# Kernel optimization log

Hardware: AMD Instinct MI355X
Metric: run time of the kernel (lower is better)

The kernel has to match this reference:

```python
import jax, jax.numpy as jnp
import numpy as np

N, NFEAT, NHID, NCLASS, NHEADS = 8192, 512, 64, 16, 4
ALPHA = 0.2          # leaky_relu slope for attention scores
OUT_SLOPE = 0.01     # flax default slope for per-head output leaky_relu
NEG = -9000000000000000.0


def glorot(key, shape):
    fan_in, fan_out = shape[0], shape[1]
    lim = jnp.sqrt(6.0 / (fan_in + fan_out))
    return jax.random.uniform(key, shape, jnp.float32, -lim, lim)


def setup_inputs() -> dict:
    key = jax.random.key(0)
    ks = jax.random.split(key, 6)
    x = jax.random.normal(ks[0], (N, NFEAT), jnp.float32)
    adj = jax.random.randint(ks[1], (N, N), 0, 2, jnp.int32)
    Wh = glorot(ks[2], (NHEADS * NFEAT, NHID)).reshape(NHEADS, NFEAT, NHID)
    ah = glorot(ks[3], (NHEADS * 2 * NHID, 1)).reshape(NHEADS, 2 * NHID, 1)
    Wo = glorot(ks[4], (NHID * NHEADS, NCLASS))
    ao = glorot(ks[5], (2 * NCLASS, 1))
    return {"x": x, "adj": adj, "Wh": Wh, "ah": ah, "Wo": Wo, "ao": ao}


def _gat_layer(x, adj_mask, W, a, score_slope):
    # h: (N, F)
    h = x @ W
    F = h.shape[1]
    # a_input[i,j] = concat(h_i, h_j); a_input @ a == f1[i] + f2[j]
    f1 = h @ a[:F, 0]   # (N,)
    f2 = h @ a[F:, 0]   # (N,)
    e = jax.nn.leaky_relu(f1[:, None] + f2[None, :], negative_slope=score_slope)
    att = jax.nn.softmax(jnp.where(adj_mask, e, NEG), axis=1)  # (N, N)
    return att @ h  # (N, F)


def reference(x, adj, Wh, ah, Wo, ao):
    adj_mask = adj > 0
    heads = []
    for k in range(NHEADS):  # small fixed structural loop
        hp = _gat_layer(x, adj_mask, Wh[k], ah[k], ALPHA)
        heads.append(jax.nn.leaky_relu(hp, negative_slope=OUT_SLOPE))
    xcat = jnp.concatenate(heads, axis=1)  # (N, NHEADS*NHID)
    # output head: concat=False -> return h_prime directly
    return _gat_layer(xcat, adj_mask, Wo, ao, ALPHA)  # (N, NCLASS)
```

## Files before the change

kernel.cpp:

```cpp
#include <hip/hip_runtime.h>
#include <stdint.h>

#define N      8192
#define FEAT   512
#define HID    64
#define NH     4
#define C1     256
#define PCH    80
#define TC     320
#define NCLS   16
#define C2     32
#define IPB    8

typedef __attribute__((ext_vector_type(8))) short bf16x8;
typedef __attribute__((ext_vector_type(4))) float f32x4;

__device__ __forceinline__ float b2f(uint16_t u){
  uint32_t x = ((uint32_t)u) << 16;
  return __builtin_bit_cast(float, x);
}
__device__ __forceinline__ uint16_t f2b(float f){
  uint32_t x = __builtin_bit_cast(uint32_t, f);
  uint32_t r = (x + 0x7fffu + ((x >> 16) & 1u)) >> 16;
  return (uint16_t)r;
}
__device__ __forceinline__ float lrelu(float v, float a){ return fmaxf(v, a * v); }

__global__ void k0_wht(const float* __restrict__ Wh, float* __restrict__ WhT){
  int idx = blockIdx.x * 256 + threadIdx.x;
  int k = idx >> 15;
  int r = idx & 32767;
  int cc = r >> 9, f = r & 511;
  WhT[idx] = Wh[k * 32768 + f * 64 + cc];
}

__global__ __launch_bounds__(256) void k1_h(const float* __restrict__ x,
    const float* __restrict__ WhT, const float* __restrict__ ah,
    uint16_t* __restrict__ H, float* __restrict__ f1, float* __restrict__ f2)
{
  __shared__ float4 xs[IPB][128];
  int t = threadIdx.x;
  int i0 = blockIdx.x * IPB;
  for (int r = t; r < IPB * 128; r += 256){
    int ii = r >> 7, o = r & 127;
    xs[ii][o] = *((const float4*)(x + (size_t)(i0 + ii) * FEAT) + o);
  }
  __syncthreads();
  int k = t >> 6, cc = t & 63;
  const float4* wrow = (const float4*)(WhT + k * 32768 + cc * 512);
  float acc[IPB] = {};
  for (int f4 = 0; f4 < 128; ++f4){
    float4 wv = wrow[f4];
    #pragma unroll
    for (int ii = 0; ii < IPB; ++ii){
      float4 xv = xs[ii][f4];
      acc[ii] += xv.x * wv.x + xv.y * wv.y + xv.z * wv.z + xv.w * wv.w;
    }
  }
  float a1 = ah[k * 128 + cc], a2 = ah[k * 128 + 64 + cc];
  #pragma unroll
  for (int ii = 0; ii < IPB; ++ii){
    int i = i0 + ii;
    H[(size_t)i * C1 + t] = f2b(acc[ii]);
    float c1v = acc[ii] * a1, c2v = acc[ii] * a2;
    #pragma unroll
    for (int off = 32; off; off >>= 1){
      c1v += __shfl_down(c1v, off);
      c2v += __shfl_down(c2v, off);
    }
    if (cc == 0){ f1[k * N + i] = c1v; f2[k * N + i] = c2v; }
  }
}

__global__ void k2a_htT(const uint16_t* __restrict__ H, uint16_t* __restrict__ HT){
  __shared__ uint16_t tile[64][65];
  int bid = blockIdx.x;
  int k = bid & 3, it = bid >> 2;
  int i0 = it * 64;
  int t = threadIdx.x;
  #pragma unroll
  for (int r = 0; r < 4; ++r){
    int ii = r * 16 + (t >> 4);
    int pp = (t & 15) * 4;
    uint2 v = *(const uint2*)(H + (size_t)(i0 + ii) * C1 + k * 64 + pp);
    const uint16_t* s = (const uint16_t*)&v;
    tile[pp + 0][ii] = s[0]; tile[pp + 1][ii] = s[1];
    tile[pp + 2][ii] = s[2]; tile[pp + 3][ii] = s[3];
  }
  __syncthreads();
  #pragma unroll
  for (int r = 0; r < 4; ++r){
    int pp = r * 16 + (t >> 4);
    int ii = (t & 15) * 4;
    uint2 v;
    uint16_t* s = (uint16_t*)&v;
    s[0] = tile[pp][ii + 0]; s[1] = tile[pp][ii + 1];
    s[2] = tile[pp][ii + 2]; s[3] = tile[pp][ii + 3];
    *(uint2*)(HT + (size_t)k * (PCH * N) + (size_t)pp * N + i0 + ii) = v;
  }
}

__global__ void k2b_fill(uint16_t* __restrict__ HT){
  int fidx = blockIdx.x * 256 + threadIdx.x;
  int k = fidx >> 14;
  int rem = fidx & 16383;
  int p = 64 + (rem >> 10);
  int i0 = (rem & 1023) << 3;
  uint32_t w = (p == 64) ? 0x3F803F80u : 0u;
  uint4 v = {w, w, w, w};
  *((uint4*)(HT + (size_t)k * (PCH * N) + (size_t)p * N + i0)) = v;
}

__global__ __launch_bounds__(256, 2) void k3_attA(const int* __restrict__ adj,
    const uint16_t* __restrict__ HT, const float* __restrict__ f1,
    const float* __restrict__ f2, float* __restrict__ accA)
{
  __shared__ uint16_t Pl[NH][64][48];
  __shared__ uint16_t Hl[TC][48];
  __shared__ float f1s[NH][64];

  const int t = threadIdx.x;
  const int ibl = blockIdx.x >> 2;
  const int js = blockIdx.x & 3;
  const int gi0 = ibl * 64;

  { int k = t >> 6, ii = t & 63; f1s[k][ii] = f1[k * N + gi0 + ii]; }

  const int tj   = t & 31;
  const int half = t >> 5;
  const int lane = t & 63;
  const int wid  = t >> 6;
  const int m    = lane & 15;
  const int q    = lane >> 4;

  f32x4 acc[4][5] = {};
  const int* arow0 = adj + (size_t)(gi0 + half) * N + tj;

  for (int jc = 0; jc < 64; ++jc){
    const int gj = js * 2048 + jc * 32;
    float f2v0 = f2[0 * N + gj + tj];
    float f2v1 = f2[1 * N + gj + tj];
    float f2v2 = f2[2 * N + gj + tj];
    float f2v3 = f2[3 * N + gj + tj];
    int av[8];
    #pragma unroll
    for (int r = 0; r < 8; ++r) av[r] = arow0[(size_t)(8 * r) * N + gj];

    __syncthreads();
    #pragma unroll
    for (int r = 0; r < 5; ++r){
      int idx = t + 256 * r;
      int p = idx >> 2, o4 = idx & 3;
      *(uint4*)&Hl[p][o4 * 8] = *(const uint4*)(HT + (size_t)p * N + gj + o4 * 8);
    }
    #pragma unroll
    for (int r = 0; r < 8; ++r){
      int i = half + 8 * r;
      int a = av[r];
      float s0 = f1s[0][i] + f2v0;
      float s1 = f1s[1][i] + f2v1;
      float s2 = f1s[2][i] + f2v2;
      float s3 = f1s[3][i] + f2v3;
      float w0 = (a > 0) ? __expf(lrelu(s0, 0.2f)) : 0.f;
      float w1 = (a > 0) ? __expf(lrelu(s1, 0.2f)) : 0.f;
      float w2 = (a > 0) ? __expf(lrelu(s2, 0.2f)) : 0.f;
      float w3 = (a > 0) ? __expf(lrelu(s3, 0.2f)) : 0.f;
      Pl[0][i][tj] = f2b(w0);
      Pl[1][i][tj] = f2b(w1);
      Pl[2][i][tj] = f2b(w2);
      Pl[3][i][tj] = f2b(w3);
    }
    __syncthreads();

    bf16x8 af[4];
    #pragma unroll
    for (int it = 0; it < 4; ++it)
      af[it] = *(const bf16x8*)&Pl[wid][it * 16 + m][q * 8];
    #pragma unroll
    for (int ct = 0; ct < 5; ++ct){
      bf16x8 bfr = *(const bf16x8*)&Hl[wid * PCH + ct * 16 + m][q * 8];
      #pragma unroll
      for (int it = 0; it < 4; ++it)
        acc[it][ct] = __builtin_amdgcn_mfma_f32_16x16x32_bf16(af[it], bfr, acc[it][ct], 0, 0, 0);
    }
  }

  #pragma unroll
  for (int it = 0; it < 4; ++it)
    #pragma unroll
    for (int ct = 0; ct < 5; ++ct)
      #pragma unroll
      for (int reg = 0; reg < 4; ++reg){
        int gi = gi0 + it * 16 + q * 4 + reg;
        int c  = wid * PCH + ct * 16 + m;
        accA[((size_t)js * N + gi) * TC + c] = acc[it][ct][reg];
      }
}

__global__ void k4_redA(const float* __restrict__ accA, uint16_t* __restrict__ xcat){
  int i = blockIdx.x;
  int t = threadIdx.x;
  int k = t >> 6, cc = t & 63;
  size_t base = (size_t)i * TC + k * PCH;
  float v = 0.f, Z = 0.f;
  #pragma unroll
  for (int js = 0; js < 4; ++js){
    const float* p = accA + (size_t)js * N * TC + base;
    v += p[cc];
    Z += p[64];
  }
  float r = v / Z;
  xcat[(size_t)i * C1 + t] = f2b(lrelu(r, 0.01f));
}

__global__ __launch_bounds__(256) void k5_h2(const uint16_t* __restrict__ xcat,
    const float* __restrict__ Wo, const float* __restrict__ ao,
    uint16_t* __restrict__ h2T, float* __restrict__ f1o, float* __restrict__ f2o)
{
  __shared__ uint16_t xs[16][256];
  int t = threadIdx.x;
  int i0 = blockIdx.x * 16;
  #pragma unroll
  for (int r = 0; r < 2; ++r){
    int idx = t + 256 * r;
    int ii = idx >> 5, o4 = idx & 31;
    *(uint4*)&xs[ii][o4 * 8] = *(const uint4*)(xcat + (size_t)(i0 + ii) * C1 + o4 * 8);
  }
  __syncthreads();
  int ii = t >> 4, c = t & 15;
  float acc = 0.f;
  for (int f = 0; f < 256; ++f)
    acc += b2f(xs[ii][f]) * Wo[f * 16 + c];
  int i = i0 + ii;
  h2T[(size_t)c * N + i] = f2b(acc);
  float u1 = acc * ao[c];
  float u2 = acc * ao[16 + c];
  #pragma unroll
  for (int off = 8; off; off >>= 1){
    u1 += __shfl_down(u1, off, 16);
    u2 += __shfl_down(u2, off, 16);
  }
  if (c == 0){ f1o[i] = u1; f2o[i] = u2; }
  if (t < 16) h2T[(size_t)16 * N + i0 + t] = 0x3F80;
  if (t < 240){
    int p = 17 + t / 16, io = t % 16;
    h2T[(size_t)p * N + i0 + io] = 0;
  }
}

__global__ __launch_bounds__(256) void k6_attB(const int* __restrict__ adj,
    const uint16_t* __restrict__ h2T, const float* __restrict__ f1o,
    const float* __restrict__ f2o, float* __restrict__ accB)
{
  __shared__ uint16_t Pl[64][48];
  __shared__ uint16_t Hl[32][48];
  __shared__ float f1s[64];

  const int t = threadIdx.x;
  const int ibl = blockIdx.x >> 3;
  const int js = blockIdx.x & 7;
  const int gi0 = ibl * 64;
  if (t < 64) f1s[t] = f1o[gi0 + t];

  const int tj = t & 31;
  const int half = t >> 5;
  const int lane = t & 63;
  const int wid = t >> 6;
  const int m = lane & 15;
  const int q = lane >> 4;

  f32x4 acc0 = {0.f, 0.f, 0.f, 0.f}, acc1 = {0.f, 0.f, 0.f, 0.f};
  const int* arow0 = adj + (size_t)(gi0 + half) * N + tj;

  for (int jc = 0; jc < 32; ++jc){
    const int gj = js * 1024 + jc * 32;
    float f2v = f2o[gj + tj];
    int av[8];
    #pragma unroll
    for (int r = 0; r < 8; ++r) av[r] = arow0[(size_t)(8 * r) * N + gj];

    __syncthreads();
    if (t < 128){
      int p = t >> 2, o4 = t & 3;
      *(uint4*)&Hl[p][o4 * 8] = *(const uint4*)(h2T + (size_t)p * N + gj + o4 * 8);
    }
    #pragma unroll
    for (int r = 0; r < 8; ++r){
      int i = half + 8 * r;
      float s = f1s[i] + f2v;
      float w = (av[r] > 0) ? __expf(lrelu(s, 0.2f)) : 0.f;
      Pl[i][tj] = f2b(w);
    }
    __syncthreads();

    bf16x8 af = *(const bf16x8*)&Pl[wid * 16 + m][q * 8];
    bf16x8 b0 = *(const bf16x8*)&Hl[m][q * 8];
    bf16x8 b1 = *(const bf16x8*)&Hl[16 + m][q * 8];
    acc0 = __builtin_amdgcn_mfma_f32_16x16x32_bf16(af, b0, acc0, 0, 0, 0);
    acc1 = __builtin_amdgcn_mfma_f32_16x16x32_bf16(af, b1, acc1, 0, 0, 0);
  }

  #pragma unroll
  for (int reg = 0; reg < 4; ++reg){
    int gi = gi0 + wid * 16 + q * 4 + reg;
    accB[((size_t)js * N + gi) * C2 + m] = acc0[reg];
    accB[((size_t)js * N + gi) * C2 + 16 + m] = acc1[reg];
  }
}

__global__ void k7_redB(const float* __restrict__ accB, float* __restrict__ out){
  int idx = blockIdx.x * 256 + threadIdx.x;
  int i = idx >> 4, c = idx & 15;
  float v = 0.f, Z = 0.f;
  #pragma unroll
  for (int js = 0; js < 8; ++js){
    const float* p = accB + ((size_t)js * N + i) * C2;
    v += p[c];
    Z += p[16];
  }
  out[idx] = v / Z;
}

extern "C" void kernel_launch(void* const* d_in, const int* in_sizes, int n_in,
                              void* d_out, int out_size, void* d_ws, size_t ws_size,
                              hipStream_t stream)
{
  const float* x   = (const float*)d_in[0];
  const int*   adj = (const int*)d_in[1];
  const float* Wh  = (const float*)d_in[2];
  const float* ah  = (const float*)d_in[3];
  const float* Wo  = (const float*)d_in[4];
  const float* ao  = (const float*)d_in[5];
  float* out = (float*)d_out;

  char* ws = (char*)d_ws;
  float*    WhT  = (float*)   (ws);
  uint16_t* H    = (uint16_t*)(ws + 524288);
  uint16_t* HT   = (uint16_t*)(ws + 4718592);
  float*    f1   = (float*)   (ws + 9961472);
  float*    f2   = (float*)   (ws + 10092544);
  float*    accA = (float*)   (ws + 10223616);
  uint16_t* xcat = (uint16_t*)(ws + 52166656);
  uint16_t* h2T  = (uint16_t*)(ws + 56360960);
  float*    f1o  = (float*)   (ws + 56885248);
  float*    f2o  = (float*)   (ws + 56918016);
  float*    accB = (float*)   (ws + 56950784);

  hipLaunchKernelGGL(k0_wht,   dim3(512),  dim3(256), 0, stream, Wh, WhT);
  hipLaunchKernelGGL(k1_h,     dim3(1024), dim3(256), 0, stream, x, WhT, ah, H, f1, f2);
  hipLaunchKernelGGL(k2a_htT,  dim3(512),  dim3(256), 0, stream, H, HT);
  hipLaunchKernelGGL(k2b_fill, dim3(256),  dim3(256), 0, stream, HT);
  hipLaunchKernelGGL(k3_attA,  dim3(512),  dim3(256), 0, stream, adj, HT, f1, f2, accA);
  hipLaunchKernelGGL(k4_redA,  dim3(8192), dim3(256), 0, stream, accA, xcat);
  hipLaunchKernelGGL(k5_h2,    dim3(512),  dim3(256), 0, stream, xcat, Wo, ao, h2T, f1o, f2o);
  hipLaunchKernelGGL(k6_attB,  dim3(1024), dim3(256), 0, stream, adj, h2T, f1o, f2o, accB);
  hipLaunchKernelGGL(k7_redB,  dim3(512),  dim3(256), 0, stream, accB, out);
}
```

Measured before the change: 630.9 us.

## Pipeline attention loads, compute softmax denominators in VALU, double block size

Both attention kernels now prefetch the next chunk's H tile, adjacency values and f2 scores into registers while computing the current chunk, using A/B register buffers. The softmax row sums are accumulated in registers and reduced with shuffles, replacing the padded ones-column in HT and dropping the fill kernel and its MFMA columns. Scores are pre-scaled by log2(e) so a native exp2 can be used, and bf16 packing goes through v_cvt_pk_bf16_f32. The first attention kernel goes to 512 threads with a head-by-row-tile wave split. The denominator is now summed from fp32 weights rather than bf16-rounded ones, which slightly changes numerics, and the extra prefetch registers may raise register pressure.

```diff
diff --git a/kernel.cpp b/kernel.cpp
--- a/kernel.cpp
+++ b/kernel.cpp
@@ -11,6 +11,7 @@
 #define NCLS   16
 #define C2     32
 #define IPB    8
+#define LOG2E  1.44269504f
 
 typedef __attribute__((ext_vector_type(8))) short bf16x8;
 typedef __attribute__((ext_vector_type(4))) float f32x4;
@@ -25,6 +26,18 @@
   return (uint16_t)r;
 }
 __device__ __forceinline__ float lrelu(float v, float a){ return fmaxf(v, a * v); }
+__device__ __forceinline__ float fexp2(float x){
+#if __has_builtin(__builtin_amdgcn_exp2f)
+  return __builtin_amdgcn_exp2f(x);
+#else
+  return exp2f(x);
+#endif
+}
+__device__ __forceinline__ uint32_t pk_bf16(float lo, float hi){
+  uint32_t r;
+  asm("v_cvt_pk_bf16_f32 %0, %1, %2" : "=v"(r) : "v"(lo), "v"(hi));
+  return r;
+}
 
 __global__ void k0_wht(const float* __restrict__ Wh, float* __restrict__ WhT){
   int idx = blockIdx.x * 256 + threadIdx.x;
@@ -68,7 +81,7 @@
       c1v += __shfl_down(c1v, off);
       c2v += __shfl_down(c2v, off);
     }
-    if (cc == 0){ f1[k * N + i] = c1v; f2[k * N + i] = c2v; }
+    if (cc == 0){ f1[k * N + i] = c1v * LOG2E; f2[k * N + i] = c2v * LOG2E; }
   }
 }
 
@@ -96,27 +109,55 @@
     uint16_t* s = (uint16_t*)&v;
     s[0] = tile[pp][ii + 0]; s[1] = tile[pp][ii + 1];
     s[2] = tile[pp][ii + 2]; s[3] = tile[pp][ii + 3];
-    *(uint2*)(HT + (size_t)k * (PCH * N) + (size_t)pp * N + i0 + ii) = v;
-  }
-}
-
-__global__ void k2b_fill(uint16_t* __restrict__ HT){
-  int fidx = blockIdx.x * 256 + threadIdx.x;
-  int k = fidx >> 14;
-  int rem = fidx & 16383;
-  int p = 64 + (rem >> 10);
-  int i0 = (rem & 1023) << 3;
-  uint32_t w = (p == 64) ? 0x3F803F80u : 0u;
-  uint4 v = {w, w, w, w};
-  *((uint4*)(HT + (size_t)k * (PCH * N) + (size_t)p * N + i0)) = v;
-}
-
-__global__ __launch_bounds__(256, 2) void k3_attA(const int* __restrict__ adj,
+    *(uint2*)(HT + (size_t)k * (64 * N) + (size_t)pp * N + i0 + ii) = v;
+  }
+}
+
+#define K3_BODY(JC, CUR, NXT)                                                    \
+  {                                                                              \
+    __syncthreads();                                                             \
+    *(uint4*)&Hl[p0][o40 * 8] = h##CUR##0;                                       \
+    *(uint4*)&Hl[p1][o40 * 8] = h##CUR##1;                                       \
+    const int gjn = js * 2048 + (((JC) + 1) & 63) * 32;                          \
+    h##NXT##0 = *(const uint4*)(src0 + gjn);                                     \
+    h##NXT##1 = *(const uint4*)(src1 + gjn);                                     \
+    _Pragma("unroll")                                                            \
+    for (int r = 0; r < 4; ++r) av##NXT[r] = arow[(size_t)(16 * r) * N + gjn];   \
+    _Pragma("unroll")                                                            \
+    for (int k = 0; k < 4; ++k) f##NXT[k] = f2[(size_t)k * N + gjn + tj];        \
+    _Pragma("unroll")                                                            \
+    for (int r = 0; r < 4; ++r){                                                 \
+      const int i = half + 16 * r;                                               \
+      const int a = av##CUR[r];                                                  \
+      float e0, e1, e2, e3;                                                      \
+      { float s = f1s[0][i] + f##CUR[0]; e0 = fexp2(fmaxf(s, 0.2f * s)); }       \
+      { float s = f1s[1][i] + f##CUR[1]; e1 = fexp2(fmaxf(s, 0.2f * s)); }       \
+      { float s = f1s[2][i] + f##CUR[2]; e2 = fexp2(fmaxf(s, 0.2f * s)); }       \
+      { float s = f1s[3][i] + f##CUR[3]; e3 = fexp2(fmaxf(s, 0.2f * s)); }       \
+      if (a <= 0){ e0 = 0.f; e1 = 0.f; e2 = 0.f; e3 = 0.f; }                     \
+      dsum[0][r] += e0; dsum[1][r] += e1;                                        \
+      dsum[2][r] += e2; dsum[3][r] += e3;                                        \
+      uint32_t pk01 = pk_bf16(e0, e1), pk23 = pk_bf16(e2, e3);                   \
+      Pl[0][i][tj] = (uint16_t)pk01; Pl[1][i][tj] = (uint16_t)(pk01 >> 16);      \
+      Pl[2][i][tj] = (uint16_t)pk23; Pl[3][i][tj] = (uint16_t)(pk23 >> 16);      \
+    }                                                                            \
+    __syncthreads();                                                             \
+    bf16x8 af0 = *(const bf16x8*)&Pl[head][(ith * 2 + 0) * 16 + m][q * 8];       \
+    bf16x8 af1 = *(const bf16x8*)&Pl[head][(ith * 2 + 1) * 16 + m][q * 8];       \
+    _Pragma("unroll")                                                            \
+    for (int ct = 0; ct < 4; ++ct){                                              \
+      bf16x8 bfr = *(const bf16x8*)&Hl[head * 64 + ct * 16 + m][q * 8];          \
+      acc[0][ct] = __builtin_amdgcn_mfma_f32_16x16x32_bf16(af0, bfr, acc[0][ct], 0, 0, 0); \
+      acc[1][ct] = __builtin_amdgcn_mfma_f32_16x16x32_bf16(af1, bfr, acc[1][ct], 0, 0, 0); \
+    }                                                                            \
+  }
+
+__global__ __launch_bounds__(512, 4) void k3_attA(const int* __restrict__ adj,
     const uint16_t* __restrict__ HT, const float* __restrict__ f1,
     const float* __restrict__ f2, float* __restrict__ accA)
 {
-  __shared__ uint16_t Pl[NH][64][48];
-  __shared__ uint16_t Hl[TC][48];
+  __shared__ uint16_t Pl[NH][64][40];
+  __shared__ uint16_t Hl[256][40];
   __shared__ float f1s[NH][64];
 
   const int t = threadIdx.x;
@@ -124,77 +165,67 @@
   const int js = blockIdx.x & 3;
   const int gi0 = ibl * 64;
 
-  { int k = t >> 6, ii = t & 63; f1s[k][ii] = f1[k * N + gi0 + ii]; }
+  if (t < 256){ int k = t >> 6, ii = t & 63; f1s[k][ii] = f1[k * N + gi0 + ii]; }
 
   const int tj   = t & 31;
   const int half = t >> 5;
   const int lane = t & 63;
-  const int wid  = t >> 6;
+  const int w    = t >> 6;
+  const int head = w >> 1;
+  const int ith  = w & 1;
   const int m    = lane & 15;
   const int q    = lane >> 4;
 
-  f32x4 acc[4][5] = {};
-  const int* arow0 = adj + (size_t)(gi0 + half) * N + tj;
-
-  for (int jc = 0; jc < 64; ++jc){
-    const int gj = js * 2048 + jc * 32;
-    float f2v0 = f2[0 * N + gj + tj];
-    float f2v1 = f2[1 * N + gj + tj];
-    float f2v2 = f2[2 * N + gj + tj];
-    float f2v3 = f2[3 * N + gj + tj];
-    int av[8];
-    #pragma unroll
-    for (int r = 0; r < 8; ++r) av[r] = arow0[(size_t)(8 * r) * N + gj];
-
-    __syncthreads();
-    #pragma unroll
-    for (int r = 0; r < 5; ++r){
-      int idx = t + 256 * r;
-      int p = idx >> 2, o4 = idx & 3;
-      *(uint4*)&Hl[p][o4 * 8] = *(const uint4*)(HT + (size_t)p * N + gj + o4 * 8);
-    }
-    #pragma unroll
-    for (int r = 0; r < 8; ++r){
-      int i = half + 8 * r;
-      int a = av[r];
-      float s0 = f1s[0][i] + f2v0;
-      float s1 = f1s[1][i] + f2v1;
-      float s2 = f1s[2][i] + f2v2;
-      float s3 = f1s[3][i] + f2v3;
-      float w0 = (a > 0) ? __expf(lrelu(s0, 0.2f)) : 0.f;
-      float w1 = (a > 0) ? __expf(lrelu(s1, 0.2f)) : 0.f;
-      float w2 = (a > 0) ? __expf(lrelu(s2, 0.2f)) : 0.f;
-      float w3 = (a > 0) ? __expf(lrelu(s3, 0.2f)) : 0.f;
-      Pl[0][i][tj] = f2b(w0);
-      Pl[1][i][tj] = f2b(w1);
-      Pl[2][i][tj] = f2b(w2);
-      Pl[3][i][tj] = f2b(w3);
-    }
-    __syncthreads();
-
-    bf16x8 af[4];
-    #pragma unroll
-    for (int it = 0; it < 4; ++it)
-      af[it] = *(const bf16x8*)&Pl[wid][it * 16 + m][q * 8];
-    #pragma unroll
-    for (int ct = 0; ct < 5; ++ct){
-      bf16x8 bfr = *(const bf16x8*)&Hl[wid * PCH + ct * 16 + m][q * 8];
-      #pragma unroll
-      for (int it = 0; it < 4; ++it)
-        acc[it][ct] = __builtin_amdgcn_mfma_f32_16x16x32_bf16(af[it], bfr, acc[it][ct], 0, 0, 0);
-    }
-  }
-
-  #pragma unroll
-  for (int it = 0; it < 4; ++it)
-    #pragma unroll
-    for (int ct = 0; ct < 5; ++ct)
+  const int p0 = t >> 2, o40 = t & 3;
+  const int p1 = p0 + 128;
+  const uint16_t* src0 = HT + (size_t)p0 * N + o40 * 8;
+  const uint16_t* src1 = HT + (size_t)p1 * N + o40 * 8;
+
+  f32x4 acc[2][4] = {};
+  float dsum[NH][4] = {};
+  const int* arow = adj + (size_t)(gi0 + half) * N + tj;
+
+  uint4 hA0, hA1, hB0, hB1;
+  int avA[4], avB[4];
+  float fA[4], fB[4];
+
+  {
+    const int gj0 = js * 2048;
+    hA0 = *(const uint4*)(src0 + gj0);
+    hA1 = *(const uint4*)(src1 + gj0);
+    #pragma unroll
+    for (int r = 0; r < 4; ++r) avA[r] = arow[(size_t)(16 * r) * N + gj0];
+    #pragma unroll
+    for (int k = 0; k < 4; ++k) fA[k] = f2[(size_t)k * N + gj0 + tj];
+  }
+
+  for (int jc = 0; jc < 64; jc += 2){
+    K3_BODY(jc,     A, B)
+    K3_BODY(jc + 1, B, A)
+  }
+
+  #pragma unroll
+  for (int itl = 0; itl < 2; ++itl)
+    #pragma unroll
+    for (int ct = 0; ct < 4; ++ct)
       #pragma unroll
       for (int reg = 0; reg < 4; ++reg){
-        int gi = gi0 + it * 16 + q * 4 + reg;
-        int c  = wid * PCH + ct * 16 + m;
-        accA[((size_t)js * N + gi) * TC + c] = acc[it][ct][reg];
+        int gi = gi0 + (ith * 2 + itl) * 16 + q * 4 + reg;
+        accA[((size_t)js * N + gi) * TC + head * PCH + ct * 16 + m] = acc[itl][ct][reg];
       }
+  #pragma unroll
+  for (int k = 0; k < 4; ++k)
+    #pragma unroll
+    for (int r = 0; r < 4; ++r){
+      float v = dsum[k][r];
+      v += __shfl_xor(v, 16);
+      v += __shfl_xor(v, 8);
+      v += __shfl_xor(v, 4);
+      v += __shfl_xor(v, 2);
+      v += __shfl_xor(v, 1);
+      if (tj == 0)
+        accA[((size_t)js * N + gi0 + half + 16 * r) * TC + k * PCH + 64] = v;
+    }
 }
 
 __global__ void k4_redA(const float* __restrict__ accA, uint16_t* __restrict__ xcat){
@@ -240,20 +271,44 @@
     u1 += __shfl_down(u1, off, 16);
     u2 += __shfl_down(u2, off, 16);
   }
-  if (c == 0){ f1o[i] = u1; f2o[i] = u2; }
-  if (t < 16) h2T[(size_t)16 * N + i0 + t] = 0x3F80;
-  if (t < 240){
-    int p = 17 + t / 16, io = t % 16;
-    h2T[(size_t)p * N + i0 + io] = 0;
-  }
-}
+  if (c == 0){ f1o[i] = u1 * LOG2E; f2o[i] = u2 * LOG2E; }
+}
+
+#define K6_BODY(JC, CUR, NXT)                                                    \
+  {                                                                              \
+    __syncthreads();                                                             \
+    if (stg) *(uint4*)&Hl[p0][o40 * 8] = h##CUR;                                 \
+    const int gjn = js * 1024 + (((JC) + 1) & 31) * 32;                          \
+    if (stg) h##NXT = *(const uint4*)(h2T + (size_t)p0 * N + gjn + o40 * 8);     \
+    _Pragma("unroll")                                                            \
+    for (int r = 0; r < 8; ++r) av##NXT[r] = arow[(size_t)(8 * r) * N + gjn];    \
+    f##NXT = f2o[gjn + tj];                                                      \
+    _Pragma("unroll")                                                            \
+    for (int rr = 0; rr < 4; ++rr){                                              \
+      const int i0r = half + 16 * rr;                                            \
+      const int i1r = i0r + 8;                                                   \
+      float s0 = f1s[i0r] + f##CUR;                                              \
+      float s1 = f1s[i1r] + f##CUR;                                              \
+      float e0 = fexp2(fmaxf(s0, 0.2f * s0));                                    \
+      float e1 = fexp2(fmaxf(s1, 0.2f * s1));                                    \
+      if (av##CUR[2 * rr]     <= 0) e0 = 0.f;                                    \
+      if (av##CUR[2 * rr + 1] <= 0) e1 = 0.f;                                    \
+      dsum[2 * rr] += e0; dsum[2 * rr + 1] += e1;                                \
+      uint32_t pk = pk_bf16(e0, e1);                                             \
+      Pl[i0r][tj] = (uint16_t)pk; Pl[i1r][tj] = (uint16_t)(pk >> 16);            \
+    }                                                                            \
+    __syncthreads();                                                             \
+    bf16x8 af = *(const bf16x8*)&Pl[wid * 16 + m][q * 8];                        \
+    bf16x8 b0 = *(const bf16x8*)&Hl[m][q * 8];                                   \
+    acc0 = __builtin_amdgcn_mfma_f32_16x16x32_bf16(af, b0, acc0, 0, 0, 0);       \
+  }
 
 __global__ __launch_bounds__(256) void k6_attB(const int* __restrict__ adj,
     const uint16_t* __restrict__ h2T, const float* __restrict__ f1o,
     const float* __restrict__ f2o, float* __restrict__ accB)
 {
-  __shared__ uint16_t Pl[64][48];
-  __shared__ uint16_t Hl[32][48];
+  __shared__ uint16_t Pl[64][40];
+  __shared__ uint16_t Hl[16][40];
   __shared__ float f1s[64];
 
   const int t = threadIdx.x;
@@ -269,42 +324,45 @@
   const int m = lane & 15;
   const int q = lane >> 4;
 
-  f32x4 acc0 = {0.f, 0.f, 0.f, 0.f}, acc1 = {0.f, 0.f, 0.f, 0.f};
-  const int* arow0 = adj + (size_t)(gi0 + half) * N + tj;
-
-  for (int jc = 0; jc < 32; ++jc){
-    const int gj = js * 1024 + jc * 32;
-    float f2v = f2o[gj + tj];
-    int av[8];
-    #pragma unroll
-    for (int r = 0; r < 8; ++r) av[r] = arow0[(size_t)(8 * r) * N + gj];
-
-    __syncthreads();
-    if (t < 128){
-      int p = t >> 2, o4 = t & 3;
-      *(uint4*)&Hl[p][o4 * 8] = *(const uint4*)(h2T + (size_t)p * N + gj + o4 * 8);
-    }
-    #pragma unroll
-    for (int r = 0; r < 8; ++r){
-      int i = half + 8 * r;
-      float s = f1s[i] + f2v;
-      float w = (av[r] > 0) ? __expf(lrelu(s, 0.2f)) : 0.f;
-      Pl[i][tj] = f2b(w);
-    }
-    __syncthreads();
-
-    bf16x8 af = *(const bf16x8*)&Pl[wid * 16 + m][q * 8];
-    bf16x8 b0 = *(const bf16x8*)&Hl[m][q * 8];
-    bf16x8 b1 = *(const bf16x8*)&Hl[16 + m][q * 8];
-    acc0 = __builtin_amdgcn_mfma_f32_16x16x32_bf16(af, b0, acc0, 0, 0, 0);
-    acc1 = __builtin_amdgcn_mfma_f32_16x16x32_bf16(af, b1, acc1, 0, 0, 0);
+  const int p0 = t >> 2, o40 = t & 3;
+  const bool stg = (t < 64);
+
+  f32x4 acc0 = {0.f, 0.f, 0.f, 0.f};
+  float dsum[8] = {};
+  const int* arow = adj + (size_t)(gi0 + half) * N + tj;
+
+  uint4 hA = {}, hB = {};
+  int avA[8], avB[8];
+  float fA, fB;
+
+  {
+    const int gj0 = js * 1024;
+    if (stg) hA = *(const uint4*)(h2T + (size_t)p0 * N + gj0 + o40 * 8);
+    #pragma unroll
+    for (int r = 0; r < 8; ++r) avA[r] = arow[(size_t)(8 * r) * N + gj0];
+    fA = f2o[gj0 + tj];
+  }
+
+  for (int jc = 0; jc < 32; jc += 2){
+    K6_BODY(jc,     A, B)
+    K6_BODY(jc + 1, B, A)
   }
 
   #pragma unroll
   for (int reg = 0; reg < 4; ++reg){
     int gi = gi0 + wid * 16 + q * 4 + reg;
     accB[((size_t)js * N + gi) * C2 + m] = acc0[reg];
-    accB[((size_t)js * N + gi) * C2 + 16 + m] = acc1[reg];
+  }
+  #pragma unroll
+  for (int r = 0; r < 8; ++r){
+    float v = dsum[r];
+    v += __shfl_xor(v, 16);
+    v += __shfl_xor(v, 8);
+    v += __shfl_xor(v, 4);
+    v += __shfl_xor(v, 2);
+    v += __shfl_xor(v, 1);
+    if (tj == 0)
+      accB[((size_t)js * N + gi0 + half + 8 * r) * C2 + 16] = v;
   }
 }
 
@@ -337,20 +395,19 @@
   float*    WhT  = (float*)   (ws);
   uint16_t* H    = (uint16_t*)(ws + 524288);
   uint16_t* HT   = (uint16_t*)(ws + 4718592);
-  float*    f1   = (float*)   (ws + 9961472);
-  float*    f2   = (float*)   (ws + 10092544);
-  float*    accA = (float*)   (ws + 10223616);
-  uint16_t* xcat = (uint16_t*)(ws + 52166656);
-  uint16_t* h2T  = (uint16_t*)(ws + 56360960);
-  float*    f1o  = (float*)   (ws + 56885248);
-  float*    f2o  = (float*)   (ws + 56918016);
-  float*    accB = (float*)   (ws + 56950784);
+  float*    f1   = (float*)   (ws + 8912896);
+  float*    f2   = (float*)   (ws + 9043968);
+  float*    accA = (float*)   (ws + 9175040);
+  uint16_t* xcat = (uint16_t*)(ws + 51118080);
+  uint16_t* h2T  = (uint16_t*)(ws + 55312384);
+  float*    f1o  = (float*)   (ws + 55574528);
+  float*    f2o  = (float*)   (ws + 55607296);
+  float*    accB = (float*)   (ws + 55640064);
 
   hipLaunchKernelGGL(k0_wht,   dim3(512),  dim3(256), 0, stream, Wh, WhT);
   hipLaunchKernelGGL(k1_h,     dim3(1024), dim3(256), 0, stream, x, WhT, ah, H, f1, f2);
   hipLaunchKernelGGL(k2a_htT,  dim3(512),  dim3(256), 0, stream, H, HT);
-  hipLaunchKernelGGL(k2b_fill, dim3(256),  dim3(256), 0, stream, HT);
-  hipLaunchKernelGGL(k3_attA,  dim3(512),  dim3(256), 0, stream, adj, HT, f1, f2, accA);
+  hipLaunchKernelGGL(k3_attA,  dim3(512),  dim3(512), 0, stream, adj, HT, f1, f2, accA);
   hipLaunchKernelGGL(k4_redA,  dim3(8192), dim3(256), 0, stream, accA, xcat);
   hipLaunchKernelGGL(k5_h2,    dim3(512),  dim3(256), 0, stream, xcat, Wo, ao, h2T, f1o, f2o);
   hipLaunchKernelGGL(k6_attB,  dim3(1024), dim3(256), 0, stream, adj, h2T, f1o, f2o, accB);
```

Measured after the change: 587.1 us. 1.07x faster.
